# Performance work log

Measured on AMD Instinct MI355X. Metric: run time of the kernel, lower is better.

## Reference

```python
import jax, jax.numpy as jnp
import numpy as np

N_NODES = 100000
N_EDGES = 3200000
D_NODE = 128
D_EDGE = 16


def setup_inputs() -> dict:
    key = jax.random.key(0)
    k1, k2, k3, k4, k5, k6, k7 = jax.random.split(key, 7)
    nodes = jax.random.normal(k1, (N_NODES, D_NODE), dtype=jnp.float32)
    edges = jax.random.normal(k2, (N_EDGES, D_EDGE), dtype=jnp.float32)
    senders = jax.random.randint(k3, (N_EDGES,), 0, N_NODES, dtype=jnp.int32)
    receivers = jax.random.randint(k4, (N_EDGES,), 0, N_NODES, dtype=jnp.int32)
    w_node = jax.random.normal(k5, (), dtype=jnp.float32)
    w_edge = jax.random.normal(k6, (), dtype=jnp.float32)
    b_node = jax.random.normal(k7, (), dtype=jnp.float32)
    return {
        "nodes": nodes,
        "edges": edges,
        "senders": senders,
        "receivers": receivers,
        "w_node": w_node,
        "w_edge": w_edge,
        "b_node": b_node,
    }


def reference(nodes, edges, senders, receivers, w_node, w_edge, b_node):
    # gather sender node scalar feature (column 0): [E]
    sender_vals = nodes[senders, 0]
    edge_vals = edges[:, 0]  # [E]
    # per-edge message: scalar mult-add
    messages = w_edge * edge_vals + w_node * sender_vals  # [E]
    # scatter-add into receivers: [N]
    agg = jax.ops.segment_sum(messages, receivers, num_segments=nodes.shape[0])
    return w_node * nodes[:, 0] + agg + b_node
```

## Files before the change

kernel.cpp:

```cpp
#include <hip/hip_runtime.h>

#define N_NODES 100000
#define N_EDGES 3200000
#define D_NODE 128
#define D_EDGE 16

#define NB 64

#define K1_THREADS 512
#define K1_EPT 8
#define K1_TILE (K1_THREADS * K1_EPT)

#define WS_X      0
#define WS_MSG    102400
#define WS_PART   (102400 + N_EDGES)
#define WS_TOTAL  (WS_PART + 4 * NB * 32768)

__global__ void tmp_k0_extract(const float* __restrict__ nodes,
                               float* __restrict__ x) {
    int i = blockIdx.x * blockDim.x + threadIdx.x;
    if (i < N_NODES) x[i] = nodes[(size_t)i * D_NODE];
}

__global__ __launch_bounds__(K1_THREADS) void tmp_k1_messages(
        const float* __restrict__ x,
        const float* __restrict__ edges,
        const int*   __restrict__ senders,
        const float* __restrict__ w_node,
        const float* __restrict__ w_edge,
        float* __restrict__ msg) {
    const float wn = w_node[0];
    const float we = w_edge[0];
    const int e0 = blockIdx.x * K1_TILE + (int)threadIdx.x * K1_EPT;
    if (e0 >= N_EDGES) return;
    int4 s0 = *(const int4*)(senders + e0);
    int4 s1 = *(const int4*)(senders + e0 + 4);
    int ss[K1_EPT] = {s0.x, s0.y, s0.z, s0.w, s1.x, s1.y, s1.z, s1.w};
    float m[K1_EPT];
#pragma unroll
    for (int j = 0; j < K1_EPT; ++j) {
        float ev = __builtin_nontemporal_load(edges + (size_t)(e0 + j) * D_EDGE);
        m[j] = we * ev + wn * x[ss[j]];
    }
    *(float4*)(msg + e0)     = make_float4(m[0], m[1], m[2], m[3]);
    *(float4*)(msg + e0 + 4) = make_float4(m[4], m[5], m[6], m[7]);
}

__global__ __launch_bounds__(1024) void tmp_k2_accum(
        const float* __restrict__ msg,
        const int*   __restrict__ receivers,
        float* __restrict__ partials,
        int range_bits) {
    extern __shared__ float acc[];
    const int range_size = 1 << range_bits;
    const int range_mask = range_size - 1;
    const int range = blockIdx.y;
    const int slice = blockIdx.x;

    for (int i = threadIdx.x; i < range_size; i += 1024) acc[i] = 0.f;
    __syncthreads();

    const int start = slice * (N_EDGES / NB);
    const int end   = start + (N_EDGES / NB);
    for (int e = start + (int)threadIdx.x * 4; e < end; e += 1024 * 4) {
        int4   r = *(const int4*)(receivers + e);
        float4 m = *(const float4*)(msg + e);
        if ((r.x >> range_bits) == range) atomicAdd(&acc[r.x & range_mask], m.x);
        if ((r.y >> range_bits) == range) atomicAdd(&acc[r.y & range_mask], m.y);
        if ((r.z >> range_bits) == range) atomicAdd(&acc[r.z & range_mask], m.z);
        if ((r.w >> range_bits) == range) atomicAdd(&acc[r.w & range_mask], m.w);
    }
    __syncthreads();

    float* dst = partials + ((size_t)(range * NB + slice) << range_bits);
    for (int i = threadIdx.x; i < range_size; i += 1024) dst[i] = acc[i];
}

__global__ void tmp_k3_reduce(const float* __restrict__ x,
                              const float* __restrict__ partials,
                              const float* __restrict__ w_node,
                              const float* __restrict__ b_node,
                              float* __restrict__ out,
                              int range_bits) {
    int i = blockIdx.x * blockDim.x + threadIdx.x;
    if (i >= N_NODES) return;
    int range = i >> range_bits;
    int local = i & ((1 << range_bits) - 1);
    float s = w_node[0] * x[i] + b_node[0];
    const float* p = partials + (((size_t)range * NB) << range_bits) + local;
#pragma unroll 4
    for (int b = 0; b < NB; ++b) s += p[(size_t)b << range_bits];
    out[i] = s;
}

__global__ void tmp_init_out(const float* __restrict__ nodes,
                             const float* __restrict__ w_node,
                             const float* __restrict__ b_node,
                             float* __restrict__ out) {
    int i = blockIdx.x * blockDim.x + threadIdx.x;
    if (i < N_NODES) out[i] = w_node[0] * nodes[(size_t)i * D_NODE] + b_node[0];
}

__global__ void tmp_edge_scatter_direct(const float* __restrict__ nodes,
                                        const float* __restrict__ edges,
                                        const int*   __restrict__ senders,
                                        const int*   __restrict__ receivers,
                                        const float* __restrict__ w_node,
                                        const float* __restrict__ w_edge,
                                        float* __restrict__ out) {
    const float wn = w_node[0];
    const float we = w_edge[0];
    int base = (blockIdx.x * blockDim.x + threadIdx.x) * 4;
    if (base + 3 < N_EDGES) {
        int4 s = *(const int4*)(senders + base);
        int4 r = *(const int4*)(receivers + base);
        atomicAdd(&out[r.x], we * edges[(size_t)(base + 0) * D_EDGE] + wn * nodes[(size_t)s.x * D_NODE]);
        atomicAdd(&out[r.y], we * edges[(size_t)(base + 1) * D_EDGE] + wn * nodes[(size_t)s.y * D_NODE]);
        atomicAdd(&out[r.z], we * edges[(size_t)(base + 2) * D_EDGE] + wn * nodes[(size_t)s.z * D_NODE]);
        atomicAdd(&out[r.w], we * edges[(size_t)(base + 3) * D_EDGE] + wn * nodes[(size_t)s.w * D_NODE]);
    } else {
        for (int e = base; e < N_EDGES; ++e) {
            atomicAdd(&out[receivers[e]],
                      we * edges[(size_t)e * D_EDGE] + wn * nodes[(size_t)senders[e] * D_NODE]);
        }
    }
}

extern "C" void kernel_launch(void* const* d_in, const int* in_sizes, int n_in,
                              void* d_out, int out_size, void* d_ws, size_t ws_size,
                              hipStream_t stream) {
    const float* nodes     = (const float*)d_in[0];
    const float* edges     = (const float*)d_in[1];
    const int*   senders   = (const int*)d_in[2];
    const int*   receivers = (const int*)d_in[3];
    const float* w_node    = (const float*)d_in[4];
    const float* w_edge    = (const float*)d_in[5];
    const float* b_node    = (const float*)d_in[6];
    float* out = (float*)d_out;
    float* ws  = (float*)d_ws;

    if (ws_size >= (size_t)WS_TOTAL * sizeof(float)) {
        float* x        = ws + WS_X;
        float* msg      = ws + WS_MSG;
        float* partials = ws + WS_PART;

        int range_bits = 15, n_ranges = 4;
        size_t lds_bytes = (size_t)(1 << range_bits) * sizeof(float);
        hipError_t attr_ok = hipFuncSetAttribute(
            reinterpret_cast<const void*>(tmp_k2_accum),
            hipFuncAttributeMaxDynamicSharedMemorySize, (int)lds_bytes);
        if (attr_ok != hipSuccess) {
            range_bits = 14; n_ranges = 7;
            lds_bytes = (size_t)(1 << range_bits) * sizeof(float);
        }

        int threads = 256;
        tmp_k0_extract<<<(N_NODES + threads - 1) / threads, threads, 0, stream>>>(
            nodes, x);

        int k1_blocks = (N_EDGES + K1_TILE - 1) / K1_TILE;
        tmp_k1_messages<<<k1_blocks, K1_THREADS, 0, stream>>>(
            x, edges, senders, w_node, w_edge, msg);

        dim3 grid2(NB, n_ranges);
        tmp_k2_accum<<<grid2, 1024, lds_bytes, stream>>>(
            msg, receivers, partials, range_bits);

        tmp_k3_reduce<<<(N_NODES + threads - 1) / threads, threads, 0, stream>>>(
            x, partials, w_node, b_node, out, range_bits);
    } else {
        int threads = 256;
        tmp_init_out<<<(N_NODES + threads - 1) / threads, threads, 0, stream>>>(
            nodes, w_node, b_node, out);
        int n_thr = N_EDGES / 4;
        tmp_edge_scatter_direct<<<(n_thr + threads - 1) / threads, threads, 0, stream>>>(
            nodes, edges, senders, receivers, w_node, w_edge, out);
    }
}
```

Measured before the change: 366.2 us.

## Use 160KB LDS node ranges, 80 edge slices, and coalesced message kernel

The LDS accumulation kernel now uses arbitrary-size node ranges (40960 floats, 160KB on MI355X), so only 3 range passes over the edge list are needed instead of 4. The slice count rises to 80 and partials are stored densely per slice with float4 writes. The message kernel switches from per-thread contiguous chunks to a strided, coalesced access pattern. The intent is to cut redundant receiver/message reads across range passes and improve occupancy balance, at the cost of a larger reduction (80 partials per node).

```diff
diff --git a/kernel.cpp b/kernel.cpp
--- a/kernel.cpp
+++ b/kernel.cpp
@@ -5,7 +5,8 @@
 #define D_NODE 128
 #define D_EDGE 16
 
-#define NB 64
+#define NB 80
+#define SLICE_E (N_EDGES / NB)
 
 #define K1_THREADS 512
 #define K1_EPT 8
@@ -14,7 +15,7 @@
 #define WS_X      0
 #define WS_MSG    102400
 #define WS_PART   (102400 + N_EDGES)
-#define WS_TOTAL  (WS_PART + 4 * NB * 32768)
+#define WS_TOTAL  (WS_PART + NB * N_NODES)
 
 __global__ void tmp_k0_extract(const float* __restrict__ nodes,
                                float* __restrict__ x) {
@@ -31,65 +32,65 @@
         float* __restrict__ msg) {
     const float wn = w_node[0];
     const float we = w_edge[0];
-    const int e0 = blockIdx.x * K1_TILE + (int)threadIdx.x * K1_EPT;
-    if (e0 >= N_EDGES) return;
-    int4 s0 = *(const int4*)(senders + e0);
-    int4 s1 = *(const int4*)(senders + e0 + 4);
-    int ss[K1_EPT] = {s0.x, s0.y, s0.z, s0.w, s1.x, s1.y, s1.z, s1.w};
-    float m[K1_EPT];
+    const int tile = blockIdx.x * K1_TILE;
 #pragma unroll
     for (int j = 0; j < K1_EPT; ++j) {
-        float ev = __builtin_nontemporal_load(edges + (size_t)(e0 + j) * D_EDGE);
-        m[j] = we * ev + wn * x[ss[j]];
+        int e = tile + j * K1_THREADS + (int)threadIdx.x;
+        if (e < N_EDGES) {
+            float ev = __builtin_nontemporal_load(edges + (size_t)e * D_EDGE);
+            int   s  = senders[e];
+            msg[e] = we * ev + wn * x[s];
+        }
     }
-    *(float4*)(msg + e0)     = make_float4(m[0], m[1], m[2], m[3]);
-    *(float4*)(msg + e0 + 4) = make_float4(m[4], m[5], m[6], m[7]);
 }
 
 __global__ __launch_bounds__(1024) void tmp_k2_accum(
         const float* __restrict__ msg,
         const int*   __restrict__ receivers,
         float* __restrict__ partials,
-        int range_bits) {
+        int range_floats) {
     extern __shared__ float acc[];
-    const int range_size = 1 << range_bits;
-    const int range_mask = range_size - 1;
-    const int range = blockIdx.y;
+    const int lo   = blockIdx.y * range_floats;
+    int span = N_NODES - lo; if (span > range_floats) span = range_floats;
+    const unsigned uspan = (unsigned)span;
     const int slice = blockIdx.x;
 
-    for (int i = threadIdx.x; i < range_size; i += 1024) acc[i] = 0.f;
+    for (int i = threadIdx.x; i < span; i += 1024) acc[i] = 0.f;
     __syncthreads();
 
-    const int start = slice * (N_EDGES / NB);
-    const int end   = start + (N_EDGES / NB);
+    const int start = slice * SLICE_E;
+    const int end   = start + SLICE_E;
     for (int e = start + (int)threadIdx.x * 4; e < end; e += 1024 * 4) {
         int4   r = *(const int4*)(receivers + e);
         float4 m = *(const float4*)(msg + e);
-        if ((r.x >> range_bits) == range) atomicAdd(&acc[r.x & range_mask], m.x);
-        if ((r.y >> range_bits) == range) atomicAdd(&acc[r.y & range_mask], m.y);
-        if ((r.z >> range_bits) == range) atomicAdd(&acc[r.z & range_mask], m.z);
-        if ((r.w >> range_bits) == range) atomicAdd(&acc[r.w & range_mask], m.w);
+        unsigned ux = (unsigned)(r.x - lo);
+        unsigned uy = (unsigned)(r.y - lo);
+        unsigned uz = (unsigned)(r.z - lo);
+        unsigned uw = (unsigned)(r.w - lo);
+        if (ux < uspan) atomicAdd(&acc[ux], m.x);
+        if (uy < uspan) atomicAdd(&acc[uy], m.y);
+        if (uz < uspan) atomicAdd(&acc[uz], m.z);
+        if (uw < uspan) atomicAdd(&acc[uw], m.w);
     }
     __syncthreads();
 
-    float* dst = partials + ((size_t)(range * NB + slice) << range_bits);
-    for (int i = threadIdx.x; i < range_size; i += 1024) dst[i] = acc[i];
+    float* dst = partials + (size_t)slice * N_NODES + lo;
+    for (int i = threadIdx.x * 4; i < span; i += 1024 * 4) {
+        *(float4*)(dst + i) = *(const float4*)(acc + i);
+    }
 }
 
 __global__ void tmp_k3_reduce(const float* __restrict__ x,
                               const float* __restrict__ partials,
                               const float* __restrict__ w_node,
                               const float* __restrict__ b_node,
-                              float* __restrict__ out,
-                              int range_bits) {
+                              float* __restrict__ out) {
     int i = blockIdx.x * blockDim.x + threadIdx.x;
     if (i >= N_NODES) return;
-    int range = i >> range_bits;
-    int local = i & ((1 << range_bits) - 1);
     float s = w_node[0] * x[i] + b_node[0];
-    const float* p = partials + (((size_t)range * NB) << range_bits) + local;
+    const float* p = partials + i;
 #pragma unroll 4
-    for (int b = 0; b < NB; ++b) s += p[(size_t)b << range_bits];
+    for (int b = 0; b < NB; ++b) s += p[(size_t)b * N_NODES];
     out[i] = s;
 }
 
@@ -144,15 +145,21 @@
         float* msg      = ws + WS_MSG;
         float* partials = ws + WS_PART;
 
-        int range_bits = 15, n_ranges = 4;
-        size_t lds_bytes = (size_t)(1 << range_bits) * sizeof(float);
-        hipError_t attr_ok = hipFuncSetAttribute(
-            reinterpret_cast<const void*>(tmp_k2_accum),
-            hipFuncAttributeMaxDynamicSharedMemorySize, (int)lds_bytes);
-        if (attr_ok != hipSuccess) {
-            range_bits = 14; n_ranges = 7;
-            lds_bytes = (size_t)(1 << range_bits) * sizeof(float);
+        int range_floats = 40960;
+        size_t lds_bytes = (size_t)range_floats * sizeof(float);
+        if (hipFuncSetAttribute(reinterpret_cast<const void*>(tmp_k2_accum),
+                                hipFuncAttributeMaxDynamicSharedMemorySize,
+                                (int)lds_bytes) != hipSuccess) {
+            range_floats = 32768;
+            lds_bytes = (size_t)range_floats * sizeof(float);
+            if (hipFuncSetAttribute(reinterpret_cast<const void*>(tmp_k2_accum),
+                                    hipFuncAttributeMaxDynamicSharedMemorySize,
+                                    (int)lds_bytes) != hipSuccess) {
+                range_floats = 16384;
+                lds_bytes = (size_t)range_floats * sizeof(float);
+            }
         }
+        int n_ranges = (N_NODES + range_floats - 1) / range_floats;
 
         int threads = 256;
         tmp_k0_extract<<<(N_NODES + threads - 1) / threads, threads, 0, stream>>>(
@@ -164,10 +171,10 @@
 
         dim3 grid2(NB, n_ranges);
         tmp_k2_accum<<<grid2, 1024, lds_bytes, stream>>>(
-            msg, receivers, partials, range_bits);
+            msg, receivers, partials, range_floats);
 
         tmp_k3_reduce<<<(N_NODES + threads - 1) / threads, threads, 0, stream>>>(
-            x, partials, w_node, b_node, out, range_bits);
+            x, partials, w_node, b_node, out);
     } else {
         int threads = 256;
         tmp_init_out<<<(N_NODES + threads - 1) / threads, threads, 0, stream>>>(
```

New measurement: 365.8 us. Within noise of the previous version (-0.1%).
